# Kernel optimization log

Measured on AMD Instinct MI355X. Metric: run time of the kernel, lower is better.

## Reference

```python
import jax, jax.numpy as jnp
import numpy as np

N, L, E, H, D = 4, 2048, 1024, 16, 64

def setup_inputs() -> dict:
    key = jax.random.key(0)
    ks = jax.random.split(key, 8)
    s = 1.0 / np.sqrt(E)
    return {
        "Q": jax.random.normal(ks[0], (N, L, E), jnp.float32),
        "K": jax.random.normal(ks[1], (N, L, E), jnp.float32),
        "V": jax.random.normal(ks[2], (N, L, E), jnp.float32),
        "Wq": jax.random.normal(ks[3], (H * D, E), jnp.float32) * s,
        "bq": jnp.zeros((H * D,), jnp.float32),
        "Wk": jax.random.normal(ks[4], (H * D, E), jnp.float32) * s,
        "bk": jnp.zeros((H * D,), jnp.float32),
        "Wv": jax.random.normal(ks[5], (H * D, E), jnp.float32) * s,
        "bv": jnp.zeros((H * D,), jnp.float32),
        "Wo": jax.random.normal(ks[6], (E, H * D), jnp.float32) * s,
        "bo": jnp.zeros((E,), jnp.float32),
    }

def reference(Q, K, V, Wq, bq, Wk, bk, Wv, bv, Wo, bo):
    n, lq, e = Q.shape
    lk = K.shape[1]
    # projections: Linear(x) = x @ W.T + b
    q = (Q @ Wq.T + bq).reshape(n, lq, H, D)
    k = (K @ Wk.T + bk).reshape(n, lk, H, D)
    v = (V @ Wv.T + bv).reshape(n, lk, H, D)
    # scores over key dim (original broadcasts Q*K and sums over d)
    scores = jnp.einsum('nqhd,nkhd->nqkh', q, k) / jnp.sqrt(jnp.float32(D))
    attn = jax.nn.softmax(scores, axis=2)  # softmax over key axis
    out = jnp.einsum('nqkh,nkhd->nqhd', attn, v)
    out = out.reshape(n, lq, H * D)
    return (out @ Wo.T + bo).reshape(n, lq, E)
```

## Files before the change

### kernel.cpp

```cpp
#include <hip/hip_runtime.h>
#include <cstdint>
#include <cstddef>


typedef __bf16 bf16x8 __attribute__((ext_vector_type(8)));
typedef __bf16 bf16x4 __attribute__((ext_vector_type(4)));
typedef float f32x4 __attribute__((ext_vector_type(4)));

#define LOG2E_OVER_SQRTD 0.18033688011112042f

__device__ __forceinline__ unsigned short f2bf(float f) {
  unsigned int u = __builtin_bit_cast(unsigned int, f);
  u = (u + 0x7fffu + ((u >> 16) & 1u)) >> 16;
  return (unsigned short)u;
}

__device__ __forceinline__ void gl2lds16(const void* g, void* l) {
  __builtin_amdgcn_global_load_lds(
      (__attribute__((address_space(1))) unsigned int*)g,
      (__attribute__((address_space(3))) unsigned int*)l, 16, 0, 0);
}

struct CvtArgs {
  const float* src[4];
  unsigned short* dst[4];
};
__global__ __launch_bounds__(256) void cvt_multi_k(CvtArgs a) {
  const float* s = a.src[blockIdx.y];
  unsigned short* d = a.dst[blockIdx.y];
  size_t i = ((size_t)blockIdx.x * 256 + threadIdx.x) * 4;
  float4 v = *(const float4*)(s + i);
  ushort4 o;
  o.x = f2bf(v.x); o.y = f2bf(v.y); o.z = f2bf(v.z); o.w = f2bf(v.w);
  *(ushort4*)(d + i) = o;
}

struct GemmDesc {
  const unsigned short* A;
  const unsigned short* Bt;
  const float* bias;
  void* C;
  int N;
  int nbx_shift;
  float scale;
  int bias_row;
  int permc;
};
struct GemmPack3 {
  GemmDesc g[3];
};

template <bool OUT_F32>
__global__ __launch_bounds__(256, 2) void gemm_multi_k(GemmPack3 p) {
  __shared__ __attribute__((aligned(16))) unsigned short As[128 * 64];
  __shared__ __attribute__((aligned(16))) unsigned short Bs[128 * 64];
  const GemmDesc d = p.g[blockIdx.x >> 9];
  const int t = blockIdx.x & 511;
  const int bx = t & ((1 << d.nbx_shift) - 1);
  const int by = t >> d.nbx_shift;

  const int tid = threadIdx.x;
  const int lane = tid & 63, wave = tid >> 6;
  const int lr = lane & 15, lg = lane >> 4;
  const int rowBase = by * 128;
  const int colBase = bx * 128;
  const int wm = (wave & 1) * 64, wn = (wave >> 1) * 64;

  f32x4 acc[4][4] = {};

  const unsigned short* gA[4];
  const unsigned short* gB[4];
  unsigned short* lA[4];
  unsigned short* lB[4];
#pragma unroll
  for (int i = 0; i < 4; ++i) {
    int s = tid + i * 256;
    int row = s >> 3;
    int c = (s & 7) ^ (row & 7);
    gA[i] = d.A + (size_t)(rowBase + row) * 1024 + c * 8;
    gB[i] = d.Bt + (size_t)(colBase + row) * 1024 + c * 8;
    lA[i] = &As[s * 8];
    lB[i] = &Bs[s * 8];
  }

  for (int kt = 0; kt < 16; ++kt) {
    const int ko = kt * 64;
#pragma unroll
    for (int i = 0; i < 4; ++i) {
      gl2lds16(gA[i] + ko, lA[i]);
      gl2lds16(gB[i] + ko, lB[i]);
    }
    __syncthreads();

#pragma unroll
    for (int ks = 0; ks < 2; ++ks) {
      bf16x8 af[4], bfr[4];
#pragma unroll
      for (int mt = 0; mt < 4; ++mt) {
        int row = wm + mt * 16 + lr;
        int c = (ks * 4 + lg) ^ (row & 7);
        af[mt] = *(const bf16x8*)&As[row * 64 + c * 8];
      }
#pragma unroll
      for (int nt = 0; nt < 4; ++nt) {
        int row = wn + nt * 16 + lr;
        int c = (ks * 4 + lg) ^ (row & 7);
        bfr[nt] = *(const bf16x8*)&Bs[row * 64 + c * 8];
      }
#pragma unroll
      for (int mt = 0; mt < 4; ++mt)
#pragma unroll
        for (int nt = 0; nt < 4; ++nt)
          acc[mt][nt] = __builtin_amdgcn_mfma_f32_16x16x32_bf16(
              af[mt], bfr[nt], acc[mt][nt], 0, 0, 0);
    }
    __syncthreads();
  }

#pragma unroll
  for (int mt = 0; mt < 4; ++mt)
#pragma unroll
    for (int nt = 0; nt < 4; ++nt) {
      int col = colBase + wn + nt * 16 + lr;
      int colStore = d.permc ? (colBase + wn + lr * 4 + nt) : col;
      float bcol = d.bias_row ? 0.f : d.bias[col];
#pragma unroll
      for (int r = 0; r < 4; ++r) {
        int row = rowBase + wm + mt * 16 + lg * 4 + r;
        float b = d.bias_row ? d.bias[row] : bcol;
        float val = (acc[mt][nt][r] + b) * d.scale;
        size_t idx = (size_t)row * (size_t)d.N + (size_t)colStore;
        if (OUT_F32)
          ((float*)d.C)[idx] = val;
        else
          ((unsigned short*)d.C)[idx] = f2bf(val);
      }
    }
}

__global__ __launch_bounds__(256, 4) void attn_k(
    const unsigned short* __restrict__ qb,
    const unsigned short* __restrict__ kb,
    const unsigned short* __restrict__ vtb,
    unsigned short* __restrict__ aob) {
  __shared__ __attribute__((aligned(16))) unsigned short Ks[64 * 64];
  __shared__ __attribute__((aligned(16))) unsigned short Vts[64 * 64];
  __shared__ __attribute__((aligned(16))) unsigned short QPs[4 * 32 * 72];

  const int tid = threadIdx.x;
  const int lane = tid & 63, wave = tid >> 6;
  const int lr = lane & 15, lg = lane >> 4;

  const int bid = blockIdx.x;
  const int qt = bid & 15;
  const int nh = bid >> 4;
  const int h = nh & 15, n = nh >> 4;
  const int q0 = qt * 128;

#pragma unroll
  for (int i = 0; i < 4; ++i) {
    int s = i * 256 + tid;
    int row = s >> 3;
    int c = (s & 7) ^ (row & 7);
    gl2lds16(qb + (((size_t)n * 2048 + q0 + row) << 10) + h * 64 + c * 8,
             &QPs[s * 8]);
  }
#pragma unroll
  for (int i = 0; i < 2; ++i) {
    int s = i * 256 + tid;
    int row = s >> 3;
    int c = (s & 7) ^ (row & 7);
    gl2lds16(kb + (((size_t)n * 2048 + row) << 10) + h * 64 + c * 8, &Ks[s * 8]);
    gl2lds16(vtb + (((size_t)(h * 64 + row)) << 13) + (size_t)n * 2048 + c * 8,
             &Vts[s * 8]);
  }
  __syncthreads();

  bf16x8 aq[2][2];
#pragma unroll
  for (int mt = 0; mt < 2; ++mt)
#pragma unroll
    for (int ks = 0; ks < 2; ++ks) {
      int row = wave * 32 + mt * 16 + lr;
      int c = (ks * 4 + lg) ^ (row & 7);
      aq[mt][ks] = *(const bf16x8*)&QPs[row * 64 + c * 8];
    }
  __syncthreads();

  unsigned short* PsW = &QPs[wave * (32 * 72)];

  f32x4 o_acc[2][4] = {};
  float lrow[2][4] = {};

  for (int kt = 0; kt < 32; ++kt) {
    f32x4 s_acc[2][4] = {};
#pragma unroll
    for (int ks = 0; ks < 2; ++ks)
#pragma unroll
      for (int nt = 0; nt < 4; ++nt) {
        int row = nt * 16 + lr;
        int c = (ks * 4 + lg) ^ (row & 7);
        bf16x8 bk = *(const bf16x8*)&Ks[row * 64 + c * 8];
#pragma unroll
        for (int mt = 0; mt < 2; ++mt)
          s_acc[mt][nt] = __builtin_amdgcn_mfma_f32_16x16x32_bf16(
              aq[mt][ks], bk, s_acc[mt][nt], 0, 0, 0);
      }

#pragma unroll
    for (int mt = 0; mt < 2; ++mt) {
      f32x4 p[4];
#pragma unroll
      for (int nt = 0; nt < 4; ++nt)
#pragma unroll
        for (int r = 0; r < 4; ++r)
          p[nt][r] = __builtin_amdgcn_exp2f(s_acc[mt][nt][r]);
#pragma unroll
      for (int r = 0; r < 4; ++r) {
        lrow[mt][r] += (p[0][r] + p[1][r]) + (p[2][r] + p[3][r]);
        f32x4 v4 = {p[0][r], p[1][r], p[2][r], p[3][r]};
        bf16x4 pk = __builtin_convertvector(v4, bf16x4);
        int prow = mt * 16 + lg * 4 + r;
        *(bf16x4*)&PsW[prow * 72 + lr * 4] = pk;
      }
    }

#pragma unroll
    for (int ks = 0; ks < 2; ++ks) {
      bf16x8 ap[2], bv[4];
#pragma unroll
      for (int mt = 0; mt < 2; ++mt)
        ap[mt] = *(const bf16x8*)&PsW[(mt * 16 + lr) * 72 + ks * 32 + lg * 8];
#pragma unroll
      for (int nt = 0; nt < 4; ++nt) {
        int row = nt * 16 + lr;
        int c = (ks * 4 + lg) ^ (row & 7);
        bv[nt] = *(const bf16x8*)&Vts[row * 64 + c * 8];
      }
#pragma unroll
      for (int mt = 0; mt < 2; ++mt)
#pragma unroll
        for (int nt = 0; nt < 4; ++nt)
          o_acc[mt][nt] = __builtin_amdgcn_mfma_f32_16x16x32_bf16(
              ap[mt], bv[nt], o_acc[mt][nt], 0, 0, 0);
    }

    __syncthreads();
    if (kt < 31) {
      const int k0 = (kt + 1) * 64;
#pragma unroll
      for (int i = 0; i < 2; ++i) {
        int s = i * 256 + tid;
        int row = s >> 3;
        int c = (s & 7) ^ (row & 7);
        gl2lds16(kb + (((size_t)n * 2048 + k0 + row) << 10) + h * 64 + c * 8,
                 &Ks[s * 8]);
        gl2lds16(vtb + (((size_t)(h * 64 + row)) << 13) + (size_t)n * 2048 +
                     k0 + c * 8,
                 &Vts[s * 8]);
      }
    }
    __syncthreads();
  }

#pragma unroll
  for (int mt = 0; mt < 2; ++mt)
#pragma unroll
    for (int r = 0; r < 4; ++r) {
      float l = lrow[mt][r];
      l += __shfl_xor(l, 1);
      l += __shfl_xor(l, 2);
      l += __shfl_xor(l, 4);
      l += __shfl_xor(l, 8);
      float inv = 1.0f / l;
      int row_l = q0 + wave * 32 + mt * 16 + lg * 4 + r;
      size_t base = (((size_t)n * 2048 + row_l) << 10) + h * 64;
#pragma unroll
      for (int nt = 0; nt < 4; ++nt)
        aob[base + nt * 16 + lr] = f2bf(o_acc[mt][nt][r] * inv);
    }
}

extern "C" void kernel_launch(void* const* d_in, const int* in_sizes, int n_in,
                              void* d_out, int out_size, void* d_ws,
                              size_t ws_size, hipStream_t stream) {
  const float* Q = (const float*)d_in[0];
  const float* K = (const float*)d_in[1];
  const float* V = (const float*)d_in[2];
  const float* Wq = (const float*)d_in[3];
  const float* bq = (const float*)d_in[4];
  const float* Wk = (const float*)d_in[5];
  const float* bk = (const float*)d_in[6];
  const float* Wv = (const float*)d_in[7];
  const float* bv = (const float*)d_in[8];
  const float* Wo = (const float*)d_in[9];
  const float* bo = (const float*)d_in[10];

  const size_t S = (size_t)8192 * 1024;
  const size_t W = (size_t)1024 * 1024;
  unsigned short* ws = (unsigned short*)d_ws;
  unsigned short* Qbf = ws;
  unsigned short* Kbf = ws + S;
  unsigned short* Vbf = ws + 2 * S;
  unsigned short* qbuf = ws + 3 * S;
  unsigned short* kbuf = ws + 4 * S;
  unsigned short* vtbuf = ws + 5 * S;
  unsigned short* Wqb = ws + 6 * S;
  unsigned short* Wkb = Wqb + W;
  unsigned short* Wvb = Wqb + 2 * W;
  unsigned short* Wob = Wqb + 3 * W;
  unsigned short* aob = Qbf;

  CvtArgs cx;
  cx.src[0] = Q; cx.dst[0] = Qbf;
  cx.src[1] = K; cx.dst[1] = Kbf;
  cx.src[2] = V; cx.dst[2] = Vbf;
  cx.src[3] = Q; cx.dst[3] = Qbf;
  cvt_multi_k<<<dim3(8192, 3), 256, 0, stream>>>(cx);

  CvtArgs cw;
  cw.src[0] = Wq; cw.dst[0] = Wqb;
  cw.src[1] = Wk; cw.dst[1] = Wkb;
  cw.src[2] = Wv; cw.dst[2] = Wvb;
  cw.src[3] = Wo; cw.dst[3] = Wob;
  cvt_multi_k<<<dim3(1024, 4), 256, 0, stream>>>(cw);

  GemmPack3 pp;
  pp.g[0] = {Qbf, Wqb, bq, qbuf, 1024, 3, LOG2E_OVER_SQRTD, 0, 0};
  pp.g[1] = {Kbf, Wkb, bk, kbuf, 1024, 3, 1.0f, 0, 0};
  pp.g[2] = {Wvb, Vbf, bv, vtbuf, 8192, 6, 1.0f, 1, 1};
  gemm_multi_k<false><<<1536, 256, 0, stream>>>(pp);

  attn_k<<<1024, 256, 0, stream>>>(qbuf, kbuf, vtbuf, aob);

  GemmPack3 po;
  po.g[0] = {aob, Wob, bo, d_out, 1024, 3, 1.0f, 0, 0};
  po.g[1] = po.g[0];
  po.g[2] = po.g[0];
  gemm_multi_k<true><<<512, 256, 0, stream>>>(po);
}
```

Measured before the change: 347.0 us.

## Restructure attention to keep P in registers via transposed S and fp16 V

Rewrites the attention kernel to compute S^T (keys as rows), so exp'd probabilities stay in registers and feed the PV MFMA directly as fp16 fragments. This removes the LDS round trip for P. Each wave now handles 64 queries held in registers, K/V tiles are double-buffered with the prefetch issued before compute, and V^T is stored as fp16. The input and weight conversions are merged into a single launch. In exchange it has higher register pressure and occupancy drops to 2 blocks, V precision changes to fp16, and there is half as many blocks.

After: 353.3 us. Within noise of the previous version (+1.8%).

```diff
diff --git a/kernel.cpp b/kernel.cpp
--- a/kernel.cpp
+++ b/kernel.cpp
@@ -6,6 +6,7 @@
 typedef __bf16 bf16x8 __attribute__((ext_vector_type(8)));
 typedef __bf16 bf16x4 __attribute__((ext_vector_type(4)));
 typedef float f32x4 __attribute__((ext_vector_type(4)));
+typedef _Float16 half4v __attribute__((ext_vector_type(4)));
 
 #define LOG2E_OVER_SQRTD 0.18033688011112042f
 
@@ -21,18 +22,26 @@
       (__attribute__((address_space(3))) unsigned int*)l, 16, 0, 0);
 }
 
-struct CvtArgs {
-  const float* src[4];
-  unsigned short* dst[4];
+struct CvtAll {
+  const float* src[7];
+  unsigned short* dst[7];
 };
-__global__ __launch_bounds__(256) void cvt_multi_k(CvtArgs a) {
-  const float* s = a.src[blockIdx.y];
-  unsigned short* d = a.dst[blockIdx.y];
-  size_t i = ((size_t)blockIdx.x * 256 + threadIdx.x) * 4;
-  float4 v = *(const float4*)(s + i);
+__global__ __launch_bounds__(256) void cvt_all_k(CvtAll a) {
+  int bid = blockIdx.x;
+  int slot, local;
+  if (bid < 24576) {
+    slot = bid >> 13;
+    local = bid & 8191;
+  } else {
+    int w = bid - 24576;
+    slot = 3 + (w >> 10);
+    local = w & 1023;
+  }
+  size_t i = ((size_t)local * 256 + threadIdx.x) * 4;
+  float4 v = *(const float4*)(a.src[slot] + i);
   ushort4 o;
   o.x = f2bf(v.x); o.y = f2bf(v.y); o.z = f2bf(v.z); o.w = f2bf(v.w);
-  *(ushort4*)(d + i) = o;
+  *(ushort4*)(a.dst[slot] + i) = o;
 }
 
 struct GemmDesc {
@@ -44,13 +53,12 @@
   int nbx_shift;
   float scale;
   int bias_row;
-  int permc;
+  int out_mode;
 };
 struct GemmPack3 {
   GemmDesc g[3];
 };
 
-template <bool OUT_F32>
 __global__ __launch_bounds__(256, 2) void gemm_multi_k(GemmPack3 p) {
   __shared__ __attribute__((aligned(16))) unsigned short As[128 * 64];
   __shared__ __attribute__((aligned(16))) unsigned short Bs[128 * 64];
@@ -122,130 +130,70 @@
 #pragma unroll
     for (int nt = 0; nt < 4; ++nt) {
       int col = colBase + wn + nt * 16 + lr;
-      int colStore = d.permc ? (colBase + wn + lr * 4 + nt) : col;
       float bcol = d.bias_row ? 0.f : d.bias[col];
 #pragma unroll
       for (int r = 0; r < 4; ++r) {
         int row = rowBase + wm + mt * 16 + lg * 4 + r;
         float b = d.bias_row ? d.bias[row] : bcol;
         float val = (acc[mt][nt][r] + b) * d.scale;
-        size_t idx = (size_t)row * (size_t)d.N + (size_t)colStore;
-        if (OUT_F32)
+        size_t idx = (size_t)row * (size_t)d.N + (size_t)col;
+        if (d.out_mode == 0)
           ((float*)d.C)[idx] = val;
+        else if (d.out_mode == 1)
+          ((unsigned short*)d.C)[idx] = f2bf(val);
         else
-          ((unsigned short*)d.C)[idx] = f2bf(val);
-      }
-    }
-}
-
-__global__ __launch_bounds__(256, 4) void attn_k(
+          ((unsigned short*)d.C)[idx] =
+              __builtin_bit_cast(unsigned short, (_Float16)val);
+      }
+    }
+}
+
+__global__ __launch_bounds__(256, 2) void attn_k(
     const unsigned short* __restrict__ qb,
     const unsigned short* __restrict__ kb,
     const unsigned short* __restrict__ vtb,
     unsigned short* __restrict__ aob) {
-  __shared__ __attribute__((aligned(16))) unsigned short Ks[64 * 64];
-  __shared__ __attribute__((aligned(16))) unsigned short Vts[64 * 64];
-  __shared__ __attribute__((aligned(16))) unsigned short QPs[4 * 32 * 72];
+  __shared__ __attribute__((aligned(16))) unsigned short Ks[2][64 * 64];
+  __shared__ __attribute__((aligned(16))) unsigned short Vts[2][64 * 64];
 
   const int tid = threadIdx.x;
   const int lane = tid & 63, wave = tid >> 6;
   const int lr = lane & 15, lg = lane >> 4;
 
   const int bid = blockIdx.x;
-  const int qt = bid & 15;
-  const int nh = bid >> 4;
+  const int qt = bid & 7;
+  const int nh = bid >> 3;
   const int h = nh & 15, n = nh >> 4;
-  const int q0 = qt * 128;
-
-#pragma unroll
-  for (int i = 0; i < 4; ++i) {
-    int s = i * 256 + tid;
-    int row = s >> 3;
-    int c = (s & 7) ^ (row & 7);
-    gl2lds16(qb + (((size_t)n * 2048 + q0 + row) << 10) + h * 64 + c * 8,
-             &QPs[s * 8]);
-  }
+  const int q0 = qt * 256;
+  const int qw = q0 + wave * 64;
+
+  bf16x8 b_q[4][2];
+#pragma unroll
+  for (int nt = 0; nt < 4; ++nt)
+#pragma unroll
+    for (int ks = 0; ks < 2; ++ks) {
+      size_t tok = (size_t)n * 2048 + qw + nt * 16 + lr;
+      b_q[nt][ks] =
+          *(const bf16x8*)(qb + (tok << 10) + h * 64 + ks * 32 + lg * 8);
+    }
+
 #pragma unroll
   for (int i = 0; i < 2; ++i) {
     int s = i * 256 + tid;
     int row = s >> 3;
     int c = (s & 7) ^ (row & 7);
-    gl2lds16(kb + (((size_t)n * 2048 + row) << 10) + h * 64 + c * 8, &Ks[s * 8]);
+    gl2lds16(kb + (((size_t)n * 2048 + row) << 10) + h * 64 + c * 8,
+             &Ks[0][s * 8]);
     gl2lds16(vtb + (((size_t)(h * 64 + row)) << 13) + (size_t)n * 2048 + c * 8,
-             &Vts[s * 8]);
+             &Vts[0][s * 8]);
   }
   __syncthreads();
 
-  bf16x8 aq[2][2];
-#pragma unroll
-  for (int mt = 0; mt < 2; ++mt)
-#pragma unroll
-    for (int ks = 0; ks < 2; ++ks) {
-      int row = wave * 32 + mt * 16 + lr;
-      int c = (ks * 4 + lg) ^ (row & 7);
-      aq[mt][ks] = *(const bf16x8*)&QPs[row * 64 + c * 8];
-    }
-  __syncthreads();
-
-  unsigned short* PsW = &QPs[wave * (32 * 72)];
-
-  f32x4 o_acc[2][4] = {};
-  float lrow[2][4] = {};
+  f32x4 o_acc[4][4] = {};
+  f32x4 lrow = {0.f, 0.f, 0.f, 0.f};
 
   for (int kt = 0; kt < 32; ++kt) {
-    f32x4 s_acc[2][4] = {};
-#pragma unroll
-    for (int ks = 0; ks < 2; ++ks)
-#pragma unroll
-      for (int nt = 0; nt < 4; ++nt) {
-        int row = nt * 16 + lr;
-        int c = (ks * 4 + lg) ^ (row & 7);
-        bf16x8 bk = *(const bf16x8*)&Ks[row * 64 + c * 8];
-#pragma unroll
-        for (int mt = 0; mt < 2; ++mt)
-          s_acc[mt][nt] = __builtin_amdgcn_mfma_f32_16x16x32_bf16(
-              aq[mt][ks], bk, s_acc[mt][nt], 0, 0, 0);
-      }
-
-#pragma unroll
-    for (int mt = 0; mt < 2; ++mt) {
-      f32x4 p[4];
-#pragma unroll
-      for (int nt = 0; nt < 4; ++nt)
-#pragma unroll
-        for (int r = 0; r < 4; ++r)
-          p[nt][r] = __builtin_amdgcn_exp2f(s_acc[mt][nt][r]);
-#pragma unroll
-      for (int r = 0; r < 4; ++r) {
-        lrow[mt][r] += (p[0][r] + p[1][r]) + (p[2][r] + p[3][r]);
-        f32x4 v4 = {p[0][r], p[1][r], p[2][r], p[3][r]};
-        bf16x4 pk = __builtin_convertvector(v4, bf16x4);
-        int prow = mt * 16 + lg * 4 + r;
-        *(bf16x4*)&PsW[prow * 72 + lr * 4] = pk;
-      }
-    }
-
-#pragma unroll
-    for (int ks = 0; ks < 2; ++ks) {
-      bf16x8 ap[2], bv[4];
-#pragma unroll
-      for (int mt = 0; mt < 2; ++mt)
-        ap[mt] = *(const bf16x8*)&PsW[(mt * 16 + lr) * 72 + ks * 32 + lg * 8];
-#pragma unroll
-      for (int nt = 0; nt < 4; ++nt) {
-        int row = nt * 16 + lr;
-        int c = (ks * 4 + lg) ^ (row & 7);
-        bv[nt] = *(const bf16x8*)&Vts[row * 64 + c * 8];
-      }
-#pragma unroll
-      for (int mt = 0; mt < 2; ++mt)
-#pragma unroll
-        for (int nt = 0; nt < 4; ++nt)
-          o_acc[mt][nt] = __builtin_amdgcn_mfma_f32_16x16x32_bf16(
-              ap[mt], bv[nt], o_acc[mt][nt], 0, 0, 0);
-    }
-
-    __syncthreads();
+    const int cur = kt & 1;
     if (kt < 31) {
       const int k0 = (kt + 1) * 64;
 #pragma unroll
@@ -254,31 +202,78 @@
         int row = s >> 3;
         int c = (s & 7) ^ (row & 7);
         gl2lds16(kb + (((size_t)n * 2048 + k0 + row) << 10) + h * 64 + c * 8,
-                 &Ks[s * 8]);
+                 &Ks[cur ^ 1][s * 8]);
         gl2lds16(vtb + (((size_t)(h * 64 + row)) << 13) + (size_t)n * 2048 +
                      k0 + c * 8,
-                 &Vts[s * 8]);
-      }
-    }
+                 &Vts[cur ^ 1][s * 8]);
+      }
+    }
+
+    half4v pfrag[4][4];
+#pragma unroll
+    for (int mt = 0; mt < 4; ++mt) {
+      bf16x8 a_k[2];
+#pragma unroll
+      for (int ks = 0; ks < 2; ++ks) {
+        int row = mt * 16 + lr;
+        int c = (ks * 4 + lg) ^ (row & 7);
+        a_k[ks] = *(const bf16x8*)&Ks[cur][row * 64 + c * 8];
+      }
+#pragma unroll
+      for (int nt = 0; nt < 4; ++nt) {
+        f32x4 s = {0.f, 0.f, 0.f, 0.f};
+        s = __builtin_amdgcn_mfma_f32_16x16x32_bf16(a_k[0], b_q[nt][0], s, 0,
+                                                    0, 0);
+        s = __builtin_amdgcn_mfma_f32_16x16x32_bf16(a_k[1], b_q[nt][1], s, 0,
+                                                    0, 0);
+        f32x4 pv;
+#pragma unroll
+        for (int r = 0; r < 4; ++r) pv[r] = __builtin_amdgcn_exp2f(s[r]);
+        lrow[nt] += (pv[0] + pv[1]) + (pv[2] + pv[3]);
+        pfrag[mt][nt] = __builtin_convertvector(pv, half4v);
+      }
+    }
+
+#pragma unroll
+    for (int kc = 0; kc < 4; ++kc) {
+      half4v a_v[4];
+#pragma unroll
+      for (int mt = 0; mt < 4; ++mt) {
+        int row = mt * 16 + lr;
+        int keyoff = kc * 16 + lg * 4;
+        int c = (keyoff >> 3) ^ (row & 7);
+        a_v[mt] = *(const half4v*)&Vts[cur][row * 64 + c * 8 + (keyoff & 7)];
+      }
+#pragma unroll
+      for (int mt = 0; mt < 4; ++mt)
+#pragma unroll
+        for (int nt = 0; nt < 4; ++nt)
+          o_acc[mt][nt] = __builtin_amdgcn_mfma_f32_16x16x16f16(
+              a_v[mt], pfrag[kc][nt], o_acc[mt][nt], 0, 0, 0);
+    }
+
     __syncthreads();
   }
 
-#pragma unroll
-  for (int mt = 0; mt < 2; ++mt)
-#pragma unroll
-    for (int r = 0; r < 4; ++r) {
-      float l = lrow[mt][r];
-      l += __shfl_xor(l, 1);
-      l += __shfl_xor(l, 2);
-      l += __shfl_xor(l, 4);
-      l += __shfl_xor(l, 8);
-      float inv = 1.0f / l;
-      int row_l = q0 + wave * 32 + mt * 16 + lg * 4 + r;
-      size_t base = (((size_t)n * 2048 + row_l) << 10) + h * 64;
-#pragma unroll
-      for (int nt = 0; nt < 4; ++nt)
-        aob[base + nt * 16 + lr] = f2bf(o_acc[mt][nt][r] * inv);
-    }
+  float inv[4];
+#pragma unroll
+  for (int nt = 0; nt < 4; ++nt) {
+    float l = lrow[nt];
+    l += __shfl_xor(l, 16);
+    l += __shfl_xor(l, 32);
+    inv[nt] = 1.0f / l;
+  }
+#pragma unroll
+  for (int nt = 0; nt < 4; ++nt) {
+    size_t tok = (size_t)n * 2048 + qw + nt * 16 + lr;
+#pragma unroll
+    for (int mt = 0; mt < 4; ++mt) {
+      f32x4 ov = o_acc[mt][nt] * inv[nt];
+      bf16x4 o4 = __builtin_convertvector(ov, bf16x4);
+      uint2 od = __builtin_bit_cast(uint2, o4);
+      *(uint2*)(aob + (tok << 10) + h * 64 + mt * 16 + lg * 4) = od;
+    }
+  }
 }
 
 extern "C" void kernel_launch(void* const* d_in, const int* in_sizes, int n_in,
@@ -311,31 +306,27 @@
   unsigned short* Wob = Wqb + 3 * W;
   unsigned short* aob = Qbf;
 
-  CvtArgs cx;
-  cx.src[0] = Q; cx.dst[0] = Qbf;
-  cx.src[1] = K; cx.dst[1] = Kbf;
-  cx.src[2] = V; cx.dst[2] = Vbf;
-  cx.src[3] = Q; cx.dst[3] = Qbf;
-  cvt_multi_k<<<dim3(8192, 3), 256, 0, stream>>>(cx);
-
-  CvtArgs cw;
-  cw.src[0] = Wq; cw.dst[0] = Wqb;
-  cw.src[1] = Wk; cw.dst[1] = Wkb;
-  cw.src[2] = Wv; cw.dst[2] = Wvb;
-  cw.src[3] = Wo; cw.dst[3] = Wob;
-  cvt_multi_k<<<dim3(1024, 4), 256, 0, stream>>>(cw);
+  CvtAll ca;
+  ca.src[0] = Q;  ca.dst[0] = Qbf;
+  ca.src[1] = K;  ca.dst[1] = Kbf;
+  ca.src[2] = V;  ca.dst[2] = Vbf;
+  ca.src[3] = Wq; ca.dst[3] = Wqb;
+  ca.src[4] = Wk; ca.dst[4] = Wkb;
+  ca.src[5] = Wv; ca.dst[5] = Wvb;
+  ca.src[6] = Wo; ca.dst[6] = Wob;
+  cvt_all_k<<<28672, 256, 0, stream>>>(ca);
 
   GemmPack3 pp;
-  pp.g[0] = {Qbf, Wqb, bq, qbuf, 1024, 3, LOG2E_OVER_SQRTD, 0, 0};
-  pp.g[1] = {Kbf, Wkb, bk, kbuf, 1024, 3, 1.0f, 0, 0};
-  pp.g[2] = {Wvb, Vbf, bv, vtbuf, 8192, 6, 1.0f, 1, 1};
-  gemm_multi_k<false><<<1536, 256, 0, stream>>>(pp);
-
-  attn_k<<<1024, 256, 0, stream>>>(qbuf, kbuf, vtbuf, aob);
+  pp.g[0] = {Qbf, Wqb, bq, qbuf, 1024, 3, LOG2E_OVER_SQRTD, 0, 1};
+  pp.g[1] = {Kbf, Wkb, bk, kbuf, 1024, 3, 1.0f, 0, 1};
+  pp.g[2] = {Wvb, Vbf, bv, vtbuf, 8192, 6, 1.0f, 1, 2};
+  gemm_multi_k<<<1536, 256, 0, stream>>>(pp);
+
+  attn_k<<<512, 256, 0, stream>>>(qbuf, kbuf, vtbuf, aob);
 
   GemmPack3 po;
   po.g[0] = {aob, Wob, bo, d_out, 1024, 3, 1.0f, 0, 0};
   po.g[1] = po.g[0];
   po.g[2] = po.g[0];
-  gemm_multi_k<true><<<512, 256, 0, stream>>>(po);
-}
+  gemm_multi_k<<<512, 256, 0, stream>>>(po);
+}
```
